# Kernel optimization log

Measured on AMD Instinct MI355X. Metric: run time of the kernel, lower is better.

## Reference

```python
import jax, jax.numpy as jnp
import numpy as np

N = 32768          # tokens per modal
TOKEN_DIM = 1024
HID_DIM = 1024
SENSE_DIM = 256
K = 512            # centroids (shared size across modals)


def setup_inputs() -> dict:
    key = jax.random.key(0)
    ks = jax.random.split(key, 10)
    s = 0.02
    return {
        "text_emb": jax.random.normal(ks[0], (N, TOKEN_DIM), jnp.float32),
        "image_emb": jax.random.normal(ks[1], (N, TOKEN_DIM), jnp.float32),
        "text_W1": jax.random.normal(ks[2], (TOKEN_DIM, HID_DIM), jnp.float32) * s,
        "text_W2": jax.random.normal(ks[3], (HID_DIM, HID_DIM), jnp.float32) * s,
        "text_W3": jax.random.normal(ks[4], (HID_DIM, SENSE_DIM), jnp.float32) * s,
        "image_W1": jax.random.normal(ks[5], (TOKEN_DIM, HID_DIM), jnp.float32) * s,
        "image_W2": jax.random.normal(ks[6], (HID_DIM, HID_DIM), jnp.float32) * s,
        "image_W3": jax.random.normal(ks[7], (HID_DIM, SENSE_DIM), jnp.float32) * s,
        "centroids_raw": jax.random.uniform(ks[8], (K, SENSE_DIM), jnp.float32),
    }


def _sense_map(x, W1, W2, W3):
    # Linear(bias=False)+Tanh x3
    h = jnp.tanh(x @ W1)
    h = jnp.tanh(h @ W2)
    return jnp.tanh(h @ W3)  # [N, sense_dim]


def _assign(se, centroids):
    # squared distance [K, N] via expansion (same math as broadcast-subtract)
    c2 = jnp.sum(centroids * centroids, axis=1)[:, None]      # [K,1]
    e2 = jnp.sum(se * se, axis=1)[None, :]                     # [1,N]
    sqdist = c2 + e2 - 2.0 * (centroids @ se.T)                # [K,N]
    # torch argmax over (sqdist.T == min) picks first min -> argmin first occurrence
    return jnp.argmin(sqdist, axis=0)                          # [N] int


def reference(text_emb, image_emb, text_W1, text_W2, text_W3,
              image_W1, image_W2, image_W3, centroids_raw):
    centroids = jnp.tanh(centroids_raw)
    se_t = _sense_map(text_emb, text_W1, text_W2, text_W3)
    se_i = _sense_map(image_emb, image_W1, image_W2, image_W3)
    sc_t = _assign(se_t, centroids)
    sc_i = _assign(se_i, centroids)

    sense_embeddings = jnp.concatenate([se_t, se_i], axis=0)   # [2N, sense_dim]
    sense_class = jnp.concatenate([sc_t, sc_i], axis=0)        # [2N]
    word_class = jnp.concatenate([jnp.zeros((N,), jnp.int32),
                                  jnp.ones((N,), jnp.int32)])

    # ragged per-sense grouping represented jit-compatibly as a stable sort
    # permutation + per-sense counts (per modal)
    order_t = jnp.argsort(sc_t, stable=True)
    order_i = jnp.argsort(sc_i, stable=True)
    counts_t = jnp.zeros((K,), jnp.int32).at[sc_t].add(1)
    counts_i = jnp.zeros((K,), jnp.int32).at[sc_i].add(1)

    return (centroids, sense_embeddings, word_class, sense_class,
            order_t, counts_t, order_i, counts_i)
```

## Files before the change

kernel.cpp:

```cpp
#include <hip/hip_runtime.h>
#include <math.h>

#define NTOK 32768
typedef unsigned short ushort_t;

#define OFF_CENT 0
#define OFF_SE   131072
#define OFF_WC   16908288
#define OFF_SC   16973824
#define OFF_OT   17039360
#define OFF_CT   17072128
#define OFF_OI   17072640
#define OFF_CI   17105408

typedef __attribute__((ext_vector_type(8))) short short8v;
typedef __attribute__((ext_vector_type(4))) float f32x4;

__device__ __forceinline__ float dot4(float4 a, float4 b){
    return a.x*b.x + a.y*b.y + a.z*b.z + a.w*b.w;
}

__device__ __forceinline__ ushort_t f2bf(float x){
    unsigned int u = __float_as_uint(x);
    unsigned int r = (u + 0x7fffu + ((u >> 16) & 1u)) >> 16;
    return (ushort_t)r;
}
__device__ __forceinline__ float bf2f(ushort_t h){
    return __uint_as_float(((unsigned int)h) << 16);
}

__device__ __forceinline__ void gload16(const void* g, void* l){
    __builtin_amdgcn_global_load_lds(
        (const __attribute__((address_space(1))) void*)g,
        (__attribute__((address_space(3))) void*)l,
        16, 0, 0);
}

__device__ __forceinline__ void cvt8(float4 a, float4 b, short8v& h, short8v& l){
    float x[8] = {a.x, a.y, a.z, a.w, b.x, b.y, b.z, b.w};
    #pragma unroll
    for (int i = 0; i < 8; ++i) {
        ushort_t hh = f2bf(x[i]);
        h[i] = (short)hh;
        l[i] = (short)f2bf(x[i] - bf2f(hh));
    }
}

__global__ __launch_bounds__(64) void k_cent(const float* __restrict__ raw,
                                             float* __restrict__ out,
                                             float* __restrict__ c2,
                                             ushort_t* __restrict__ ch,
                                             ushort_t* __restrict__ cl)
{
    int c = blockIdx.x, l = threadIdx.x;
    float4 v = *(const float4*)(raw + (size_t)c*256 + l*4);
    float4 t;
    t.x = tanhf(v.x); t.y = tanhf(v.y); t.z = tanhf(v.z); t.w = tanhf(v.w);
    *(float4*)(out + OFF_CENT + (size_t)c*256 + l*4) = t;
    ushort4 h = make_ushort4(f2bf(t.x), f2bf(t.y), f2bf(t.z), f2bf(t.w));
    ushort4 lo = make_ushort4(f2bf(t.x - bf2f(h.x)), f2bf(t.y - bf2f(h.y)),
                              f2bf(t.z - bf2f(h.z)), f2bf(t.w - bf2f(h.w)));
    *(ushort4*)(ch + (size_t)c*256 + l*4) = h;
    *(ushort4*)(cl + (size_t)c*256 + l*4) = lo;
    float s = dot4(t, t);
    #pragma unroll
    for (int off = 32; off > 0; off >>= 1) s += __shfl_down(s, off);
    if (l == 0) c2[c] = s;
}

__global__ __launch_bounds__(256) void k_esplit(const float* __restrict__ x,
                                                ushort_t* __restrict__ hi,
                                                ushort_t* __restrict__ lo,
                                                long n4)
{
    long g = (long)blockIdx.x*256 + threadIdx.x;
    if (g >= n4) return;
    float4 v = ((const float4*)x)[g];
    ushort_t h0 = f2bf(v.x), h1 = f2bf(v.y), h2 = f2bf(v.z), h3 = f2bf(v.w);
    ushort4 h = make_ushort4(h0, h1, h2, h3);
    ushort4 l = make_ushort4(f2bf(v.x - bf2f(h0)), f2bf(v.y - bf2f(h1)),
                             f2bf(v.z - bf2f(h2)), f2bf(v.w - bf2f(h3)));
    ((ushort4*)hi)[g] = h;
    ((ushort4*)lo)[g] = l;
}

__device__ __forceinline__ void wsplit_tile(const float* __restrict__ W,
                                            ushort_t* __restrict__ Wt_hi,
                                            ushort_t* __restrict__ Wt_lo,
                                            int K, int N, int bx, int by)
{
    __shared__ float t[32][33];
    int k0 = by*32, n0 = bx*32;
    int tx = threadIdx.x & 31, ty = threadIdx.x >> 5;
    #pragma unroll
    for (int r = 0; r < 4; ++r)
        t[ty + r*8][tx] = W[(size_t)(k0 + ty + r*8)*N + n0 + tx];
    __syncthreads();
    #pragma unroll
    for (int r = 0; r < 4; ++r) {
        int n = ty + r*8;
        float x = t[tx][n];
        ushort_t h = f2bf(x);
        Wt_hi[(size_t)(n0+n)*K + k0 + tx] = h;
        Wt_lo[(size_t)(n0+n)*K + k0 + tx] = f2bf(x - bf2f(h));
    }
}

__global__ __launch_bounds__(256) void k_prep(
    const float* __restrict__ W1t, const float* __restrict__ W2t, const float* __restrict__ W3t,
    const float* __restrict__ W1i, const float* __restrict__ W2i, const float* __restrict__ W3i,
    ushort_t* __restrict__ wreg, float* __restrict__ out)
{
    const size_t WM = 4*1048576 + 2*262144;
    int b = blockIdx.x;
    if (b >= 4608) {
        int g = (b - 4608)*256 + threadIdx.x;
        float v = (g*4 < NTOK) ? 0.f : 1.f;
        ((float4*)(out + OFF_WC))[g] = make_float4(v, v, v, v);
        return;
    }
    int m = b / 2304;
    int r = b % 2304;
    ushort_t* base = wreg + (size_t)m*WM;
    const float* Ws[3][2] = {{W1t, W1i}, {W2t, W2i}, {W3t, W3i}};
    if (r < 1024) {
        wsplit_tile(Ws[0][m], base, base + 1048576, 1024, 1024, r % 32, r / 32);
    } else if (r < 2048) {
        int r2 = r - 1024;
        wsplit_tile(Ws[1][m], base + 2*1048576, base + 3*1048576, 1024, 1024, r2 % 32, r2 / 32);
    } else {
        int r3 = r - 2048;
        wsplit_tile(Ws[2][m], base + 4*1048576, base + 4*1048576 + 262144, 1024, 256, r3 % 8, r3 / 8);
    }
}

__global__ __launch_bounds__(512, 2) void k_gemm_l1(
    const float* __restrict__ Af, const ushort_t* __restrict__ Bt_hi,
    ushort_t* __restrict__ C_hi, ushort_t* __restrict__ C_lo,
    unsigned bDelta, int N)
{
    __shared__ ushort_t lds[65536];

    const int tid  = threadIdx.x;
    const int wave = tid >> 6, lane = tid & 63;
    const int wr = wave >> 2, wc = wave & 3;
    const int fr = lane & 15, fq = lane >> 4;

    int nwg = gridDim.x;
    int id = blockIdx.x;
    if (!(nwg & 7)) { int cpx = nwg >> 3; id = (id & 7)*cpx + (id >> 3); }
    const int nx = N >> 8;
    const int n0 = (id % nx) * 256;
    const int m0 = (id / nx) * 256;

    const int srow0 = tid >> 2;
    const int qx = (tid & 3) ^ ((srow0 >> 1) & 3);

    const float* fA0 = Af + (size_t)(m0 + srow0) * 1024 + qx*8;
    const float* fA1 = fA0 + 131072;
    const unsigned offB0 = (unsigned)(n0 + srow0) * 1024u + (unsigned)qx * 8u;
    const ushort_t* pB0  = Bt_hi + offB0;
    const ushort_t* pB1  = pB0 + 131072u;
    const ushort_t* pB0l = pB0 + bDelta;
    const ushort_t* pB1l = pB1 + bDelta;
    const unsigned ldsS0 = (unsigned)wave * 512u;
    const unsigned ldsS1 = ldsS0 + 4096u;
    const unsigned wOff  = ldsS0 + (unsigned)lane * 8u;

    const unsigned fb = (unsigned)fr*32u + (unsigned)((fq ^ ((fr >> 1) & 3)) * 8);
    const ushort_t* p0 = lds + fb;
    const ushort_t* p1 = p0 + 32768u;

    f32x4 acc[8][4] = {};

#define STGB(KT, WB) { \
    unsigned wb_ = (unsigned)(WB) * 32768u; \
    gload16(pB0  + (KT), lds + wb_ + 16384u + ldsS0); \
    gload16(pB1  + (KT), lds + wb_ + 16384u + ldsS1); \
    gload16(pB0l + (KT), lds + wb_ + 24576u + ldsS0); \
    gload16(pB1l + (KT), lds + wb_ + 24576u + ldsS1); \
}
#define RA1(P, hl, i) (*(const short8v*)((P) + (hl)*8192u + (unsigned)wr*4096u + (unsigned)(i)*512u))
#define RB1(P, hl, j) (*(const short8v*)((P) + 16384u + (hl)*8192u + (unsigned)wc*2048u + (unsigned)(j)*512u))
#define MM16(A8, B8, C4) __builtin_amdgcn_mfma_f32_16x16x32_bf16(A8, B8, C4, 0, 0, 0)

    {
        float4 a00 = *(const float4*)(fA0);
        float4 a01 = *(const float4*)(fA0 + 4);
        float4 a10 = *(const float4*)(fA1);
        float4 a11 = *(const float4*)(fA1 + 4);
        STGB(0, 0);
        short8v h0, l0, h1, l1;
        cvt8(a00, a01, h0, l0);
        cvt8(a10, a11, h1, l1);
        *(short8v*)(lds + wOff)          = h0;
        *(short8v*)(lds + 4096u + wOff)  = h1;
        *(short8v*)(lds + 8192u + wOff)  = l0;
        *(short8v*)(lds + 12288u + wOff) = l1;
    }
    __syncthreads();

    #pragma unroll 1
    for (int kt = 0; kt < 1024; kt += 32) {
        const int par = (kt >> 5) & 1;
        const ushort_t* cp = par ? p1 : p0;
        const bool pf = (kt + 32) < 1024;

        float4 a00, a01, a10, a11;
        if (pf) {
            a00 = *(const float4*)(fA0 + kt + 32);
            a01 = *(const float4*)(fA0 + kt + 36);
            a10 = *(const float4*)(fA1 + kt + 32);
            a11 = *(const float4*)(fA1 + kt + 36);
            STGB(kt + 32, par ^ 1);
        }

        short8v bh0 = RB1(cp,0,0), bl0 = RB1(cp,1,0);
        short8v bh1 = RB1(cp,0,1), bl1 = RB1(cp,1,1);
        short8v bh2 = RB1(cp,0,2), bl2 = RB1(cp,1,2);
        short8v bh3 = RB1(cp,0,3), bl3 = RB1(cp,1,3);

        __builtin_amdgcn_s_setprio(1);
        #pragma unroll
        for (int i = 0; i < 8; ++i) {
            short8v ah = RA1(cp,0,i), al = RA1(cp,1,i);
            acc[i][0] = MM16(ah, bh0, acc[i][0]);
            acc[i][1] = MM16(ah, bh1, acc[i][1]);
            acc[i][2] = MM16(ah, bh2, acc[i][2]);
            acc[i][3] = MM16(ah, bh3, acc[i][3]);
            acc[i][0] = MM16(ah, bl0, acc[i][0]);
            acc[i][1] = MM16(ah, bl1, acc[i][1]);
            acc[i][2] = MM16(ah, bl2, acc[i][2]);
            acc[i][3] = MM16(ah, bl3, acc[i][3]);
            acc[i][0] = MM16(al, bh0, acc[i][0]);
            acc[i][1] = MM16(al, bh1, acc[i][1]);
            acc[i][2] = MM16(al, bh2, acc[i][2]);
            acc[i][3] = MM16(al, bh3, acc[i][3]);
        }
        __builtin_amdgcn_s_setprio(0);

        if (pf) {
            unsigned wb = (unsigned)(par ^ 1) * 32768u;
            short8v h0, l0, h1, l1;
            cvt8(a00, a01, h0, l0);
            cvt8(a10, a11, h1, l1);
            *(short8v*)(lds + wb + wOff)          = h0;
            *(short8v*)(lds + wb + 4096u + wOff)  = h1;
            *(short8v*)(lds + wb + 8192u + wOff)  = l0;
            *(short8v*)(lds + wb + 12288u + wOff) = l1;
        }
        __syncthreads();
    }

    #pragma unroll
    for (int i = 0; i < 8; ++i)
        #pragma unroll
        for (int j = 0; j < 4; ++j)
            #pragma unroll
            for (int r = 0; r < 4; ++r) {
                int row = m0 + wr*128 + i*16 + fq*4 + r;
                int col = n0 + wc*64 + j*16 + fr;
                float t = tanhf(acc[i][j][r]);
                size_t idx = (size_t)row*N + col;
                ushort_t h = f2bf(t);
                C_hi[idx] = h;
                C_lo[idx] = f2bf(t - bf2f(h));
            }
#undef STGB
#undef RA1
#undef RB1
#undef MM16
}

__global__ __launch_bounds__(512, 2) void k_gemm_mfma256(
    const ushort_t* __restrict__ A_hi, const ushort_t* __restrict__ Bt_hi,
    ushort_t* __restrict__ C_hi, ushort_t* __restrict__ C_lo,
    unsigned aDelta, unsigned bDelta, int N)
{
    __shared__ ushort_t lds[65536];

    const int tid  = threadIdx.x;
    const int wave = tid >> 6, lane = tid & 63;
    const int wr = wave >> 2, wc = wave & 3;
    const int fr = lane & 15, fq = lane >> 4;

    int nwg = gridDim.x;
    int id = blockIdx.x;
    if (!(nwg & 7)) { int cpx = nwg >> 3; id = (id & 7)*cpx + (id >> 3); }
    const int nx = N >> 8;
    const int n0 = (id % nx) * 256;
    const int m0 = (id / nx) * 256;

    const int srow0 = tid >> 2;
    const int qx = (tid & 3) ^ ((srow0 >> 1) & 3);

    const unsigned offA0 = (unsigned)(m0 + srow0) * 1024u + (unsigned)qx * 8u;
    const unsigned offB0 = (unsigned)(n0 + srow0) * 1024u + (unsigned)qx * 8u;
    const ushort_t* pA0  = A_hi + offA0;
    const ushort_t* pA1  = pA0 + 131072u;
    const ushort_t* pA0l = pA0 + aDelta;
    const ushort_t* pA1l = pA1 + aDelta;
    const ushort_t* pB0  = Bt_hi + offB0;
    const ushort_t* pB1  = pB0 + 131072u;
    const ushort_t* pB0l = pB0 + bDelta;
    const ushort_t* pB1l = pB1 + bDelta;
    const unsigned ldsS0 = (unsigned)wave * 512u;
    const unsigned ldsS1 = ldsS0 + 4096u;

    const unsigned fb = (unsigned)fr*32u + (unsigned)((fq ^ ((fr >> 1) & 3)) * 8);
    const ushort_t* p0 = lds + fb;
    const ushort_t* p1 = p0 + 32768u;

    f32x4 acc[8][4] = {};

#define STG(KT, WB) { \
    unsigned wb_ = (unsigned)(WB) * 32768u; \
    gload16(pA0  + (KT), lds + wb_ +           ldsS0); \
    gload16(pA1  + (KT), lds + wb_ +           ldsS1); \
    gload16(pA0l + (KT), lds + wb_ +  8192u +  ldsS0); \
    gload16(pA1l + (KT), lds + wb_ +  8192u +  ldsS1); \
    gload16(pB0  + (KT), lds + wb_ + 16384u +  ldsS0); \
    gload16(pB1  + (KT), lds + wb_ + 16384u +  ldsS1); \
    gload16(pB0l + (KT), lds + wb_ + 24576u +  ldsS0); \
    gload16(pB1l + (KT), lds + wb_ + 24576u +  ldsS1); \
}
#define RA(P, hl, i) (*(const short8v*)((P) + (hl)*8192u + (unsigned)wr*4096u + (unsigned)(i)*512u))
#define RB(P, hl, j) (*(const short8v*)((P) + 16384u + (hl)*8192u + (unsigned)wc*2048u + (unsigned)(j)*512u))
#define MM16(A8, B8, C4) __builtin_amdgcn_mfma_f32_16x16x32_bf16(A8, B8, C4, 0, 0, 0)

    STG(0, 0);
    __syncthreads();

    #pragma unroll 1
    for (int kt = 0; kt < 1024; kt += 32) {
        const int par = (kt >> 5) & 1;
        const ushort_t* cp = par ? p1 : p0;

        short8v bh0 = RB(cp,0,0), bl0 = RB(cp,1,0);
        short8v bh1 = RB(cp,0,1), bl1 = RB(cp,1,1);
        short8v bh2 = RB(cp,0,2), bl2 = RB(cp,1,2);
        short8v bh3 = RB(cp,0,3), bl3 = RB(cp,1,3);

        if (kt + 32 < 1024) STG(kt + 32, par ^ 1);

        __builtin_amdgcn_s_setprio(1);
        #pragma unroll
        for (int i = 0; i < 8; ++i) {
            short8v ah = RA(cp,0,i), al = RA(cp,1,i);
            acc[i][0] = MM16(ah, bh0, acc[i][0]);
            acc[i][1] = MM16(ah, bh1, acc[i][1]);
            acc[i][2] = MM16(ah, bh2, acc[i][2]);
            acc[i][3] = MM16(ah, bh3, acc[i][3]);
            acc[i][0] = MM16(ah, bl0, acc[i][0]);
            acc[i][1] = MM16(ah, bl1, acc[i][1]);
            acc[i][2] = MM16(ah, bl2, acc[i][2]);
            acc[i][3] = MM16(ah, bl3, acc[i][3]);
            acc[i][0] = MM16(al, bh0, acc[i][0]);
            acc[i][1] = MM16(al, bh1, acc[i][1]);
            acc[i][2] = MM16(al, bh2, acc[i][2]);
            acc[i][3] = MM16(al, bh3, acc[i][3]);
        }
        __builtin_amdgcn_s_setprio(0);

        __syncthreads();
    }

    #pragma unroll
    for (int i = 0; i < 8; ++i)
        #pragma unroll
        for (int j = 0; j < 4; ++j)
            #pragma unroll
            for (int r = 0; r < 4; ++r) {
                int row = m0 + wr*128 + i*16 + fq*4 + r;
                int col = n0 + wc*64 + j*16 + fr;
                float t = tanhf(acc[i][j][r]);
                size_t idx = (size_t)row*N + col;
                ushort_t h = f2bf(t);
                C_hi[idx] = h;
                C_lo[idx] = f2bf(t - bf2f(h));
            }
#undef STG
#undef RA
#undef RB
#undef MM16
}

__global__ __launch_bounds__(256, 2) void k_gemm_mfma(
    const ushort_t* __restrict__ A_hi, const ushort_t* __restrict__ A_lo,
    const ushort_t* __restrict__ Bt_hi, const ushort_t* __restrict__ Bt_lo,
    ushort_t* __restrict__ C_hi, ushort_t* __restrict__ C_lo,
    float* __restrict__ Cf,
    int N)
{
    __shared__ ushort_t lds[32768];

    const int tid  = threadIdx.x;
    const int wave = tid >> 6, lane = tid & 63;
    const int wr = wave >> 1, wc = wave & 1;
    const int fr = lane & 15, fq = lane >> 4;

    int nwg = gridDim.x * gridDim.y;
    int id = blockIdx.y * gridDim.x + blockIdx.x;
    if (!(nwg & 7)) { int cpx = nwg >> 3; id = (id & 7)*cpx + (id >> 3); }
    const int m0 = (id / gridDim.x) * 128, n0 = (id % gridDim.x) * 128;

    const int sl = lane >> 2;
    const int sq = (lane & 3) ^ ((sl >> 1) & 3);
    const unsigned ga0 = (unsigned)(m0 + wave*32 + sl) * 1024u + (unsigned)sq * 8u;
    const unsigned gb0 = (unsigned)(n0 + wave*32 + sl) * 1024u + (unsigned)sq * 8u;
    const ushort_t* pa0 = A_hi  + ga0;       const ushort_t* pa1 = pa0 + 16384u;
    const ushort_t* pal0 = A_lo + ga0;       const ushort_t* pal1 = pal0 + 16384u;
    const ushort_t* pb0 = Bt_hi + gb0;       const ushort_t* pb1 = pb0 + 16384u;
    const ushort_t* pbl0 = Bt_lo + gb0;      const ushort_t* pbl1 = pbl0 + 16384u;
    const unsigned sl0 = (unsigned)wave * 1024u;
    const unsigned sl1 = sl0 + 512u;

    const unsigned fb = (unsigned)fr*32u + (unsigned)((fq ^ ((fr >> 1) & 3)) * 8);
    const ushort_t* q0 = lds + fb;
    const ushort_t* q1 = q0 + 16384u;

    f32x4 acc[4][4] = {};

#define STG3(KT, WB) { \
    unsigned wb_ = (unsigned)(WB) * 16384u; \
    gload16(pa0  + (KT), lds + wb_ +           sl0); \
    gload16(pa1  + (KT), lds + wb_ +           sl1); \
    gload16(pal0 + (KT), lds + wb_ +  4096u +  sl0); \
    gload16(pal1 + (KT), lds + wb_ +  4096u +  sl1); \
    gload16(pb0  + (KT), lds + wb_ +  8192u +  sl0); \
    gload16(pb1  + (KT), lds + wb_ +  8192u +  sl1); \
    gload16(pbl0 + (KT), lds + wb_ + 12288u +  sl0); \
    gload16(pbl1 + (KT), lds + wb_ + 12288u +  sl1); \
}
#define RA3(P, hl, i) (*(const short8v*)((P) + (hl)*4096u + (unsigned)wr*2048u + (unsigned)(i)*512u))
#define RB3(P, hl, j) (*(const short8v*)((P) + 8192u + (hl)*4096u + (unsigned)wc*2048u + (unsigned)(j)*512u))
#define MM16(A8, B8, C4) __builtin_amdgcn_mfma_f32_16x16x32_bf16(A8, B8, C4, 0, 0, 0)

    STG3(0, 0);
    __syncthreads();

    #pragma unroll 1
    for (int kt = 0; kt < 1024; kt += 32) {
        const int par = (kt >> 5) & 1;
        const ushort_t* cp = par ? q1 : q0;

        short8v bh0 = RB3(cp,0,0), bl0 = RB3(cp,1,0);
        short8v bh1 = RB3(cp,0,1), bl1 = RB3(cp,1,1);
        short8v bh2 = RB3(cp,0,2), bl2 = RB3(cp,1,2);
        short8v bh3 = RB3(cp,0,3), bl3 = RB3(cp,1,3);

        if (kt + 32 < 1024) STG3(kt + 32, par ^ 1);

        __builtin_amdgcn_s_setprio(1);
        #pragma unroll
        for (int i = 0; i < 4; ++i) {
            short8v ah = RA3(cp,0,i), al = RA3(cp,1,i);
            acc[i][0] = MM16(ah, bh0, acc[i][0]);
            acc[i][1] = MM16(ah, bh1, acc[i][1]);
            acc[i][2] = MM16(ah, bh2, acc[i][2]);
            acc[i][3] = MM16(ah, bh3, acc[i][3]);
            acc[i][0] = MM16(ah, bl0, acc[i][0]);
            acc[i][1] = MM16(ah, bl1, acc[i][1]);
            acc[i][2] = MM16(ah, bl2, acc[i][2]);
            acc[i][3] = MM16(ah, bl3, acc[i][3]);
            acc[i][0] = MM16(al, bh0, acc[i][0]);
            acc[i][1] = MM16(al, bh1, acc[i][1]);
            acc[i][2] = MM16(al, bh2, acc[i][2]);
            acc[i][3] = MM16(al, bh3, acc[i][3]);
        }
        __builtin_amdgcn_s_setprio(0);

        __syncthreads();
    }

    #pragma unroll
    for (int i = 0; i < 4; ++i)
        #pragma unroll
        for (int j = 0; j < 4; ++j)
            #pragma unroll
            for (int r = 0; r < 4; ++r) {
                int row = m0 + wr*64 + i*16 + fq*4 + r;
                int col = n0 + wc*64 + j*16 + fr;
                float t = tanhf(acc[i][j][r]);
                size_t idx = (size_t)row*N + col;
                if (Cf) Cf[idx] = t;
                if (C_hi) {
                    ushort_t h = f2bf(t);
                    C_hi[idx] = h;
                    C_lo[idx] = f2bf(t - bf2f(h));
                }
            }
#undef STG3
#undef RA3
#undef RB3
#undef MM16
}

__global__ __launch_bounds__(256) void k_assign_mfma(
    const ushort_t* __restrict__ SEh, const ushort_t* __restrict__ SEl,
    const ushort_t* __restrict__ ch, const ushort_t* __restrict__ cl,
    const float* __restrict__ c2,
    int* __restrict__ sc, float* __restrict__ out_w,
    int* __restrict__ blockHist)
{
    __shared__ ushort_t lds[16384];
    __shared__ float c2s[512];
    __shared__ float redD[128][2];
    __shared__ int   redI[128][2];

    const int modal = blockIdx.y;
    const int t0 = blockIdx.x * 128;
    const int tid  = threadIdx.x;
    const int wave = tid >> 6, lane = tid & 63;
    const int wr = wave >> 1, wc = wave & 1;
    const int fr = lane & 15, fq = lane >> 4;

    const ushort_t* seh = SEh + (size_t)modal * NTOK * 256;
    const ushort_t* sel = SEl + (size_t)modal * NTOK * 256;

    c2s[tid] = c2[tid];
    c2s[tid + 256] = c2[tid + 256];

    int srow[2], sq[2], slbase[2];
    #pragma unroll
    for (int r = 0; r < 2; ++r) {
        int row = wave*32 + r*16 + (lane >> 2);
        srow[r]   = row;
        sq[r]     = (lane & 3) ^ ((row >> 1) & 3);
        slbase[r] = wave*1024 + r*512;
    }

    float bd[16]; int bi[16];
    #pragma unroll
    for (int s = 0; s < 16; ++s) { bd[s] = 3.4e38f; bi[s] = 0; }

    for (int j = 0; j < 4; ++j) {
        f32x4 acc[4][4] = {};
        for (int kt = 0; kt < 256; kt += 32) {
            __syncthreads();
            #pragma unroll
            for (int r = 0; r < 2; ++r) {
                size_t ga = (size_t)(t0 + srow[r]) * 256 + kt + sq[r]*8;
                size_t gc = (size_t)(j*128 + srow[r]) * 256 + kt + sq[r]*8;
                gload16(seh + ga, lds          + slbase[r]);
                gload16(sel + ga, lds + 4096   + slbase[r]);
                gload16(ch  + gc, lds + 8192   + slbase[r]);
                gload16(cl  + gc, lds + 12288  + slbase[r]);
            }
            __syncthreads();

            short8v ah[4], al[4], bh[4], bl[4];
            #pragma unroll
            for (int i = 0; i < 4; ++i) {
                int rowa = wr*64 + i*16 + fr;
                int offa = rowa*32 + ((fq ^ ((rowa >> 1) & 3)) * 8);
                ah[i] = *(const short8v*)(lds + offa);
                al[i] = *(const short8v*)(lds + 4096 + offa);
                int rowb = wc*64 + i*16 + fr;
                int offb = rowb*32 + ((fq ^ ((rowb >> 1) & 3)) * 8);
                bh[i] = *(const short8v*)(lds + 8192 + offb);
                bl[i] = *(const short8v*)(lds + 12288 + offb);
            }
            #pragma unroll
            for (int i = 0; i < 4; ++i)
                #pragma unroll
                for (int jj = 0; jj < 4; ++jj) {
                    acc[i][jj] = __builtin_amdgcn_mfma_f32_16x16x32_bf16(ah[i], bh[jj], acc[i][jj], 0, 0, 0);
                    acc[i][jj] = __builtin_amdgcn_mfma_f32_16x16x32_bf16(ah[i], bl[jj], acc[i][jj], 0, 0, 0);
                    acc[i][jj] = __builtin_amdgcn_mfma_f32_16x16x32_bf16(al[i], bh[jj], acc[i][jj], 0, 0, 0);
                }
        }
        #pragma unroll
        for (int i = 0; i < 4; ++i)
            #pragma unroll
            for (int jj = 0; jj < 4; ++jj) {
                int col = j*128 + wc*64 + jj*16 + fr;
                float cc = c2s[col];
                #pragma unroll
                for (int r = 0; r < 4; ++r) {
                    float d = cc - 2.f * acc[i][jj][r];
                    int s = i*4 + r;
                    if (d < bd[s]) { bd[s] = d; bi[s] = col; }
                }
            }
    }

    #pragma unroll
    for (int s = 0; s < 16; ++s) {
        #pragma unroll
        for (int off = 1; off < 16; off <<= 1) {
            float od = __shfl_xor(bd[s], off);
            int   oi = __shfl_xor(bi[s], off);
            if (od < bd[s] || (od == bd[s] && oi < bi[s])) { bd[s] = od; bi[s] = oi; }
        }
    }
    if (fr == 0) {
        #pragma unroll
        for (int i = 0; i < 4; ++i)
            #pragma unroll
            for (int r = 0; r < 4; ++r) {
                int tl = wr*64 + i*16 + fq*4 + r;
                redD[tl][wc] = bd[i*4 + r];
                redI[tl][wc] = bi[i*4 + r];
            }
    }
    __syncthreads();
    if (tid < 128) {
        float d0 = redD[tid][0], d1 = redD[tid][1];
        int   i0 = redI[tid][0], i1 = redI[tid][1];
        if (d1 < d0 || (d1 == d0 && i1 < i0)) { d0 = d1; i0 = i1; }
        int g = t0 + tid;
        sc[modal*NTOK + g] = i0;
        out_w[OFF_SC + (size_t)modal*NTOK + g] = (float)i0;
        atomicAdd(&blockHist[(modal*128 + (g >> 8))*512 + i0], 1);
    }
}

__global__ __launch_bounds__(256) void k_assign(
    const float* __restrict__ out_ro,
    const float* __restrict__ c2,
    int* __restrict__ sc,
    float* __restrict__ out_w,
    int* __restrict__ blockHist)
{
    const int modal = blockIdx.y;
    const int tok0 = blockIdx.x * 64;
    const float* se   = out_ro + OFF_SE + (size_t)modal * NTOK * 256;
    const float* cent = out_ro + OFF_CENT;

    __shared__ float4 se4[64][64];
    __shared__ float4 ct4[64][64];

    const int tid = threadIdx.x;
    const int tt = tid & 15, cc = tid >> 4;

    {
        int rbase = tid >> 6;
        int d4 = tid & 63;
        #pragma unroll
        for (int i = 0; i < 16; ++i) {
            int t = i*4 + rbase;
            float4 v = *(const float4*)(se + (size_t)(tok0 + t)*256 + d4*4);
            se4[t][d4 ^ (t >> 2)] = v;
        }
    }
    __syncthreads();

    float e2r[4];
    #pragma unroll
    for (int k2 = 0; k2 < 4; ++k2) {
        float s = 0.f;
        for (int d4 = 0; d4 < 64; ++d4) {
            float4 v = se4[4*tt + k2][d4 ^ tt];
            s += dot4(v, v);
        }
        e2r[k2] = s;
    }

    float bd[4]; int bi[4];
    #pragma unroll
    for (int k2 = 0; k2 < 4; ++k2) { bd[k2] = 3.4e38f; bi[k2] = 0; }

    for (int ctile = 0; ctile < 8; ++ctile) {
        int c0 = ctile * 64;
        {
            int rbase = tid >> 6;
            int d4 = tid & 63;
            #pragma unroll
            for (int i = 0; i < 16; ++i) {
                int r = i*4 + rbase;
                float4 v = *(const float4*)(cent + (size_t)(c0 + r)*256 + d4*4);
                ct4[r][d4 ^ (r >> 2)] = v;
            }
        }
        __syncthreads();

        float accd[4][4];
        #pragma unroll
        for (int a = 0; a < 4; ++a)
            #pragma unroll
            for (int b = 0; b < 4; ++b) accd[a][b] = 0.f;

        for (int d4 = 0; d4 < 64; ++d4) {
            float4 sv[4], cv[4];
            #pragma unroll
            for (int k2 = 0; k2 < 4; ++k2) sv[k2] = se4[4*tt + k2][d4 ^ tt];
            #pragma unroll
            for (int jx = 0; jx < 4; ++jx) cv[jx] = ct4[4*cc + jx][d4 ^ cc];
            #pragma unroll
            for (int k2 = 0; k2 < 4; ++k2)
                #pragma unroll
                for (int jx = 0; jx < 4; ++jx)
                    accd[k2][jx] += dot4(sv[k2], cv[jx]);
        }

        #pragma unroll
        for (int jx = 0; jx < 4; ++jx) {
            int cidx = c0 + 4*cc + jx;
            float cj = c2[cidx];
            #pragma unroll
            for (int k2 = 0; k2 < 4; ++k2) {
                float d = cj + e2r[k2] - 2.f * accd[k2][jx];
                if (d < bd[k2]) { bd[k2] = d; bi[k2] = cidx; }
            }
        }
        __syncthreads();
    }

    float* red_d = (float*)ct4;
    int*   red_i = (int*)ct4 + 64*17;
    #pragma unroll
    for (int k2 = 0; k2 < 4; ++k2) {
        red_d[(4*tt + k2)*17 + cc] = bd[k2];
        red_i[(4*tt + k2)*17 + cc] = bi[k2];
    }
    __syncthreads();
    if (tid < 64) {
        float b = red_d[tid*17]; int ix = red_i[tid*17];
        #pragma unroll
        for (int q = 1; q < 16; ++q) {
            float d = red_d[tid*17 + q]; int i2 = red_i[tid*17 + q];
            if (d < b || (d == b && i2 < ix)) { b = d; ix = i2; }
        }
        int g = tok0 + tid;
        sc[modal*NTOK + g] = ix;
        out_w[OFF_SC + (size_t)modal*NTOK + g] = (float)ix;
        atomicAdd(&blockHist[(modal*128 + (g >> 8))*512 + ix], 1);
    }
}

__global__ __launch_bounds__(512) void k_scan(const int* __restrict__ blockHist,
                                              int* __restrict__ blockBase,
                                              int* __restrict__ classBase,
                                              float* __restrict__ out)
{
    int modal = blockIdx.x;
    int c = threadIdx.x;
    int run = 0;
    for (int b = 0; b < 128; ++b) {
        int idx = (modal*128 + b)*512 + c;
        blockBase[idx] = run;
        run += blockHist[idx];
    }
    float* cnt = out + (modal ? OFF_CI : OFF_CT);
    cnt[c] = (float)run;

    __shared__ int s[512];
    s[c] = run;
    __syncthreads();
    int total = run;
    for (int off = 1; off < 512; off <<= 1) {
        int v = 0;
        if (c >= off) v = s[c - off];
        __syncthreads();
        s[c] += v;
        __syncthreads();
    }
    classBase[modal*512 + c] = s[c] - total;
}

__global__ __launch_bounds__(256) void k_scatter(const int* __restrict__ sc,
                                                 const int* __restrict__ blockBase,
                                                 const int* __restrict__ classBase,
                                                 float* __restrict__ out)
{
    int modal = blockIdx.y, blk = blockIdx.x, tid = threadIdx.x;
    __shared__ int cls[256];
    int t = blk*256 + tid;
    int c = sc[modal*NTOK + t];
    cls[tid] = c;
    __syncthreads();
    int rank = 0;
    for (int j = 0; j < tid; ++j) rank += (cls[j] == c) ? 1 : 0;
    int pos = classBase[modal*512 + c] + blockBase[(modal*128 + blk)*512 + c] + rank;
    float* oo = out + (modal ? OFF_OI : OFF_OT);
    oo[pos] = (float)t;
}

extern "C" void kernel_launch(void* const* d_in, const int* in_sizes, int n_in,
                              void* d_out, int out_size, void* d_ws, size_t ws_size,
                              hipStream_t stream)
{
    const float* text_emb  = (const float*)d_in[0];
    const float* image_emb = (const float*)d_in[1];
    const float* W[2][3] = {
        {(const float*)d_in[2], (const float*)d_in[3], (const float*)d_in[4]},
        {(const float*)d_in[5], (const float*)d_in[6], (const float*)d_in[7]}
    };
    const float* cent_raw = (const float*)d_in[8];
    float* out = (float*)d_out;
    char* w = (char*)d_ws;

    int*   sc        = (int*)w;
    int*   blockHist = (int*)(w + 0x40000);
    int*   blockBase = (int*)(w + 0xC0000);
    int*   classBase = (int*)(w + 0x140000);
    float* c2        = (float*)(w + 0x141000);
    ushort_t* cent_h = (ushort_t*)(w + 0x142000);
    ushort_t* cent_l = (ushort_t*)(w + 0x182000);

    ushort_t* wreg = (ushort_t*)(w + 0x200000);
    const size_t WM = 4*1048576 + 2*262144;

    ushort_t* SEh = (ushort_t*)(w + 0x1400000);
    ushort_t* SEl = (ushort_t*)(w + 0x3400000);

    bool mfmaAssign = true;
    size_t actoff = 0x5400000;
    int Mc = 0;
    for (int c = NTOK; c >= 256; c >>= 1)
        if (actoff + (size_t)c*8192 <= ws_size) { Mc = c; break; }
    if (Mc == 0) {
        mfmaAssign = false;
        actoff = 0x1400000;
        for (int c = NTOK; c >= 256; c >>= 1)
            if (actoff + (size_t)c*8192 <= ws_size) { Mc = c; break; }
        if (Mc == 0) Mc = 256;
    }
    ushort_t* act = (ushort_t*)(w + actoff);

    hipMemsetAsync(blockHist, 0, 2*128*512*sizeof(int), stream);

    k_cent<<<dim3(512), dim3(64), 0, stream>>>(cent_raw, out, c2, cent_h, cent_l);
    k_prep<<<dim3(4672), dim3(256), 0, stream>>>(
        W[0][0], W[0][1], W[0][2], W[1][0], W[1][1], W[1][2], wreg, out);

    for (int m = 0; m < 2; ++m) {
        const float* emb = m ? image_emb : text_emb;
        ushort_t* w1h = wreg + (size_t)m*WM;
        ushort_t* w2h = w1h + 2*1048576;
        ushort_t* w3h = w1h + 4*1048576;
        ushort_t* w3l = w3h + 262144;

        ushort_t* Ah = act;
        ushort_t* Al = Ah + (size_t)Mc*1024;
        ushort_t* Hh = Al + (size_t)Mc*1024;
        ushort_t* Hl = Hh + (size_t)Mc*1024;

        for (int s0 = 0; s0 < NTOK; s0 += Mc) {
            k_gemm_l1<<<dim3((Mc/256)*4), dim3(512), 0, stream>>>(
                emb + (size_t)s0*1024, w1h, Hh, Hl, 1048576u, 1024);
            k_gemm_mfma256<<<dim3((Mc/256)*4), dim3(512), 0, stream>>>(
                Hh, w2h, Ah, Al, (unsigned)Mc*1024u, 1048576u, 1024);
            ushort_t* seh_ptr = mfmaAssign ? SEh + ((size_t)m*NTOK + s0)*256 : nullptr;
            ushort_t* sel_ptr = mfmaAssign ? SEl + ((size_t)m*NTOK + s0)*256 : nullptr;
            k_gemm_mfma<<<dim3(2, Mc/128), dim3(256), 0, stream>>>(
                Ah, Al, w3h, w3l, seh_ptr, sel_ptr,
                out + OFF_SE + ((size_t)m*NTOK + s0)*256, 256);
        }
    }

    if (mfmaAssign) {
        k_assign_mfma<<<dim3(256, 2), dim3(256), 0, stream>>>(
            SEh, SEl, cent_h, cent_l, c2, sc, out, blockHist);
    } else {
        k_assign<<<dim3(512, 2), dim3(256), 0, stream>>>(out, c2, sc, out, blockHist);
    }
    k_scan   <<<dim3(2),      dim3(512), 0, stream>>>(blockHist, blockBase, classBase, out);
    k_scatter<<<dim3(128, 2), dim3(256), 0, stream>>>(sc, blockBase, classBase, out);
}
```

Measured before the change: 1.030 ms.

## Double-buffer assign MFMA loads, fuse centroid prep, parallelize histogram scan

The assign kernel now runs one flattened 32-step loop with double-buffered LDS, so global-to-LDS loads for the next tile overlap the MFMA work on the current one and one barrier per step is removed. Centroid tanh and split is folded into k_prep as extra blocks, removing a separate launch. The serial 128-step per-class scan is split into a parallel wave-shuffle scan across blocks followed by a small class-prefix kernel. LDS use in the assign kernel doubles, which may lower occupancy.

```diff
diff --git a/kernel.cpp b/kernel.cpp
--- a/kernel.cpp
+++ b/kernel.cpp
@@ -44,28 +44,6 @@
         h[i] = (short)hh;
         l[i] = (short)f2bf(x[i] - bf2f(hh));
     }
-}
-
-__global__ __launch_bounds__(64) void k_cent(const float* __restrict__ raw,
-                                             float* __restrict__ out,
-                                             float* __restrict__ c2,
-                                             ushort_t* __restrict__ ch,
-                                             ushort_t* __restrict__ cl)
-{
-    int c = blockIdx.x, l = threadIdx.x;
-    float4 v = *(const float4*)(raw + (size_t)c*256 + l*4);
-    float4 t;
-    t.x = tanhf(v.x); t.y = tanhf(v.y); t.z = tanhf(v.z); t.w = tanhf(v.w);
-    *(float4*)(out + OFF_CENT + (size_t)c*256 + l*4) = t;
-    ushort4 h = make_ushort4(f2bf(t.x), f2bf(t.y), f2bf(t.z), f2bf(t.w));
-    ushort4 lo = make_ushort4(f2bf(t.x - bf2f(h.x)), f2bf(t.y - bf2f(h.y)),
-                              f2bf(t.z - bf2f(h.z)), f2bf(t.w - bf2f(h.w)));
-    *(ushort4*)(ch + (size_t)c*256 + l*4) = h;
-    *(ushort4*)(cl + (size_t)c*256 + l*4) = lo;
-    float s = dot4(t, t);
-    #pragma unroll
-    for (int off = 32; off > 0; off >>= 1) s += __shfl_down(s, off);
-    if (l == 0) c2[c] = s;
 }
 
 __global__ __launch_bounds__(256) void k_esplit(const float* __restrict__ x,
@@ -109,10 +87,30 @@
 __global__ __launch_bounds__(256) void k_prep(
     const float* __restrict__ W1t, const float* __restrict__ W2t, const float* __restrict__ W3t,
     const float* __restrict__ W1i, const float* __restrict__ W2i, const float* __restrict__ W3i,
-    ushort_t* __restrict__ wreg, float* __restrict__ out)
+    ushort_t* __restrict__ wreg, float* __restrict__ out,
+    const float* __restrict__ cent_raw, float* __restrict__ c2,
+    ushort_t* __restrict__ ch, ushort_t* __restrict__ cl)
 {
     const size_t WM = 4*1048576 + 2*262144;
     int b = blockIdx.x;
+    if (b >= 4672) {
+        int c = (b - 4672)*4 + (threadIdx.x >> 6);
+        int l = threadIdx.x & 63;
+        float4 v = *(const float4*)(cent_raw + (size_t)c*256 + l*4);
+        float4 t;
+        t.x = tanhf(v.x); t.y = tanhf(v.y); t.z = tanhf(v.z); t.w = tanhf(v.w);
+        *(float4*)(out + OFF_CENT + (size_t)c*256 + l*4) = t;
+        ushort4 h = make_ushort4(f2bf(t.x), f2bf(t.y), f2bf(t.z), f2bf(t.w));
+        ushort4 lo = make_ushort4(f2bf(t.x - bf2f(h.x)), f2bf(t.y - bf2f(h.y)),
+                                  f2bf(t.z - bf2f(h.z)), f2bf(t.w - bf2f(h.w)));
+        *(ushort4*)(ch + (size_t)c*256 + l*4) = h;
+        *(ushort4*)(cl + (size_t)c*256 + l*4) = lo;
+        float s = dot4(t, t);
+        #pragma unroll
+        for (int off = 32; off > 0; off >>= 1) s += __shfl_down(s, off);
+        if (l == 0) c2[c] = s;
+        return;
+    }
     if (b >= 4608) {
         int g = (b - 4608)*256 + threadIdx.x;
         float v = (g*4 < NTOK) ? 0.f : 1.f;
@@ -503,7 +501,7 @@
     int* __restrict__ sc, float* __restrict__ out_w,
     int* __restrict__ blockHist)
 {
-    __shared__ ushort_t lds[16384];
+    __shared__ ushort_t lds[32768];
     __shared__ float c2s[512];
     __shared__ float redD[128][2];
     __shared__ int   redI[128][2];
@@ -521,69 +519,92 @@
     c2s[tid] = c2[tid];
     c2s[tid + 256] = c2[tid + 256];
 
-    int srow[2], sq[2], slbase[2];
-    #pragma unroll
-    for (int r = 0; r < 2; ++r) {
-        int row = wave*32 + r*16 + (lane >> 2);
-        srow[r]   = row;
-        sq[r]     = (lane & 3) ^ ((row >> 1) & 3);
-        slbase[r] = wave*1024 + r*512;
-    }
+    const int sl = lane >> 2;
+    const int sq = (lane & 3) ^ ((sl >> 1) & 3);
+    const unsigned sA = (unsigned)(t0 + wave*32 + sl) * 256u + (unsigned)sq * 8u;
+    const unsigned sC = (unsigned)(wave*32 + sl) * 256u + (unsigned)sq * 8u;
+    const ushort_t* pse0 = seh + sA;   const ushort_t* pse1 = pse0 + 4096u;
+    const ushort_t* psl0 = sel + sA;   const ushort_t* psl1 = psl0 + 4096u;
+    const ushort_t* pch0 = ch + sC;    const ushort_t* pch1 = pch0 + 4096u;
+    const ushort_t* pcl0 = cl + sC;    const ushort_t* pcl1 = pcl0 + 4096u;
+    const unsigned d0 = (unsigned)wave * 1024u;
+    const unsigned d1 = d0 + 512u;
+
+#define STA(S, BUF) { \
+    int j_ = (S) >> 3; unsigned kt_ = (unsigned)((S) & 7) * 32u; \
+    unsigned bb = (unsigned)(BUF) * 16384u; \
+    unsigned co = (unsigned)j_*32768u + kt_; \
+    gload16(pse0 + kt_, lds + bb +           d0); \
+    gload16(pse1 + kt_, lds + bb +           d1); \
+    gload16(psl0 + kt_, lds + bb +  4096u +  d0); \
+    gload16(psl1 + kt_, lds + bb +  4096u +  d1); \
+    gload16(pch0 + co,  lds + bb +  8192u +  d0); \
+    gload16(pch1 + co,  lds + bb +  8192u +  d1); \
+    gload16(pcl0 + co,  lds + bb + 12288u +  d0); \
+    gload16(pcl1 + co,  lds + bb + 12288u +  d1); \
+}
 
     float bd[16]; int bi[16];
     #pragma unroll
     for (int s = 0; s < 16; ++s) { bd[s] = 3.4e38f; bi[s] = 0; }
 
-    for (int j = 0; j < 4; ++j) {
-        f32x4 acc[4][4] = {};
-        for (int kt = 0; kt < 256; kt += 32) {
-            __syncthreads();
-            #pragma unroll
-            for (int r = 0; r < 2; ++r) {
-                size_t ga = (size_t)(t0 + srow[r]) * 256 + kt + sq[r]*8;
-                size_t gc = (size_t)(j*128 + srow[r]) * 256 + kt + sq[r]*8;
-                gload16(seh + ga, lds          + slbase[r]);
-                gload16(sel + ga, lds + 4096   + slbase[r]);
-                gload16(ch  + gc, lds + 8192   + slbase[r]);
-                gload16(cl  + gc, lds + 12288  + slbase[r]);
+    STA(0, 0);
+    __syncthreads();
+
+    f32x4 acc[4][4];
+    #pragma unroll 1
+    for (int s = 0; s < 32; ++s) {
+        const int j = s >> 3;
+        const ushort_t* cp = lds + (unsigned)(s & 1) * 16384u;
+
+        if ((s & 7) == 0) {
+            #pragma unroll
+            for (int i = 0; i < 4; ++i)
+                #pragma unroll
+                for (int jj = 0; jj < 4; ++jj) acc[i][jj] = (f32x4){0.f,0.f,0.f,0.f};
+        }
+
+        if (s + 1 < 32) STA(s + 1, (s & 1) ^ 1);
+
+        short8v ah[4], al[4], bh[4], bl[4];
+        #pragma unroll
+        for (int i = 0; i < 4; ++i) {
+            int rowa = wr*64 + i*16 + fr;
+            int offa = rowa*32 + ((fq ^ ((rowa >> 1) & 3)) * 8);
+            ah[i] = *(const short8v*)(cp + offa);
+            al[i] = *(const short8v*)(cp + 4096 + offa);
+            int rowb = wc*64 + i*16 + fr;
+            int offb = rowb*32 + ((fq ^ ((rowb >> 1) & 3)) * 8);
+            bh[i] = *(const short8v*)(cp + 8192 + offb);
+            bl[i] = *(const short8v*)(cp + 12288 + offb);
+        }
+        #pragma unroll
+        for (int i = 0; i < 4; ++i)
+            #pragma unroll
+            for (int jj = 0; jj < 4; ++jj) {
+                acc[i][jj] = __builtin_amdgcn_mfma_f32_16x16x32_bf16(ah[i], bh[jj], acc[i][jj], 0, 0, 0);
+                acc[i][jj] = __builtin_amdgcn_mfma_f32_16x16x32_bf16(ah[i], bl[jj], acc[i][jj], 0, 0, 0);
+                acc[i][jj] = __builtin_amdgcn_mfma_f32_16x16x32_bf16(al[i], bh[jj], acc[i][jj], 0, 0, 0);
             }
-            __syncthreads();
-
-            short8v ah[4], al[4], bh[4], bl[4];
-            #pragma unroll
-            for (int i = 0; i < 4; ++i) {
-                int rowa = wr*64 + i*16 + fr;
-                int offa = rowa*32 + ((fq ^ ((rowa >> 1) & 3)) * 8);
-                ah[i] = *(const short8v*)(lds + offa);
-                al[i] = *(const short8v*)(lds + 4096 + offa);
-                int rowb = wc*64 + i*16 + fr;
-                int offb = rowb*32 + ((fq ^ ((rowb >> 1) & 3)) * 8);
-                bh[i] = *(const short8v*)(lds + 8192 + offb);
-                bl[i] = *(const short8v*)(lds + 12288 + offb);
-            }
+
+        if ((s & 7) == 7) {
             #pragma unroll
             for (int i = 0; i < 4; ++i)
                 #pragma unroll
                 for (int jj = 0; jj < 4; ++jj) {
-                    acc[i][jj] = __builtin_amdgcn_mfma_f32_16x16x32_bf16(ah[i], bh[jj], acc[i][jj], 0, 0, 0);
-                    acc[i][jj] = __builtin_amdgcn_mfma_f32_16x16x32_bf16(ah[i], bl[jj], acc[i][jj], 0, 0, 0);
-                    acc[i][jj] = __builtin_amdgcn_mfma_f32_16x16x32_bf16(al[i], bh[jj], acc[i][jj], 0, 0, 0);
+                    int col = j*128 + wc*64 + jj*16 + fr;
+                    float cc = c2s[col];
+                    #pragma unroll
+                    for (int r = 0; r < 4; ++r) {
+                        float d = cc - 2.f * acc[i][jj][r];
+                        int si = i*4 + r;
+                        if (d < bd[si]) { bd[si] = d; bi[si] = col; }
+                    }
                 }
         }
-        #pragma unroll
-        for (int i = 0; i < 4; ++i)
-            #pragma unroll
-            for (int jj = 0; jj < 4; ++jj) {
-                int col = j*128 + wc*64 + jj*16 + fr;
-                float cc = c2s[col];
-                #pragma unroll
-                for (int r = 0; r < 4; ++r) {
-                    float d = cc - 2.f * acc[i][jj][r];
-                    int s = i*4 + r;
-                    if (d < bd[s]) { bd[s] = d; bi[s] = col; }
-                }
-            }
-    }
+        __syncthreads();
+    }
+#undef STA
 
     #pragma unroll
     for (int s = 0; s < 16; ++s) {
@@ -606,9 +627,9 @@
     }
     __syncthreads();
     if (tid < 128) {
-        float d0 = redD[tid][0], d1 = redD[tid][1];
+        float dd0 = redD[tid][0], dd1 = redD[tid][1];
         int   i0 = redI[tid][0], i1 = redI[tid][1];
-        if (d1 < d0 || (d1 == d0 && i1 < i0)) { d0 = d1; i0 = i1; }
+        if (dd1 < dd0 || (dd1 == dd0 && i1 < i0)) { dd0 = dd1; i0 = i1; }
         int g = t0 + tid;
         sc[modal*NTOK + g] = i0;
         out_w[OFF_SC + (size_t)modal*NTOK + g] = (float)i0;
@@ -729,26 +750,38 @@
     }
 }
 
-__global__ __launch_bounds__(512) void k_scan(const int* __restrict__ blockHist,
-                                              int* __restrict__ blockBase,
-                                              int* __restrict__ classBase,
-                                              float* __restrict__ out)
+__global__ __launch_bounds__(128) void k_scan1(const int* __restrict__ blockHist,
+                                               int* __restrict__ blockBase,
+                                               int* __restrict__ classTot)
+{
+    int c = blockIdx.x, modal = blockIdx.y, t = threadIdx.x;
+    __shared__ int wsum;
+    int v = blockHist[(modal*128 + t)*512 + c];
+    int incl = v;
+    #pragma unroll
+    for (int off = 1; off < 64; off <<= 1) {
+        int u = __shfl_up(incl, off);
+        if ((t & 63) >= off) incl += u;
+    }
+    if (t == 63) wsum = incl;
+    __syncthreads();
+    if (t >= 64) incl += wsum;
+    blockBase[(modal*128 + t)*512 + c] = incl - v;
+    if (t == 127) classTot[modal*512 + c] = incl;
+}
+
+__global__ __launch_bounds__(512) void k_scan2(int* __restrict__ classBase,
+                                               float* __restrict__ out)
 {
     int modal = blockIdx.x;
     int c = threadIdx.x;
-    int run = 0;
-    for (int b = 0; b < 128; ++b) {
-        int idx = (modal*128 + b)*512 + c;
-        blockBase[idx] = run;
-        run += blockHist[idx];
-    }
+    int total = classBase[modal*512 + c];
     float* cnt = out + (modal ? OFF_CI : OFF_CT);
-    cnt[c] = (float)run;
+    cnt[c] = (float)total;
 
     __shared__ int s[512];
-    s[c] = run;
-    __syncthreads();
-    int total = run;
+    s[c] = total;
+    __syncthreads();
     for (int off = 1; off < 512; off <<= 1) {
         int v = 0;
         if (c >= off) v = s[c - off];
@@ -821,9 +854,9 @@
 
     hipMemsetAsync(blockHist, 0, 2*128*512*sizeof(int), stream);
 
-    k_cent<<<dim3(512), dim3(64), 0, stream>>>(cent_raw, out, c2, cent_h, cent_l);
-    k_prep<<<dim3(4672), dim3(256), 0, stream>>>(
-        W[0][0], W[0][1], W[0][2], W[1][0], W[1][1], W[1][2], wreg, out);
+    k_prep<<<dim3(4800), dim3(256), 0, stream>>>(
+        W[0][0], W[0][1], W[0][2], W[1][0], W[1][1], W[1][2], wreg, out,
+        cent_raw, c2, cent_h, cent_l);
 
     for (int m = 0; m < 2; ++m) {
         const float* emb = m ? image_emb : text_emb;
@@ -856,6 +889,7 @@
     } else {
         k_assign<<<dim3(512, 2), dim3(256), 0, stream>>>(out, c2, sc, out, blockHist);
     }
-    k_scan   <<<dim3(2),      dim3(512), 0, stream>>>(blockHist, blockBase, classBase, out);
+    k_scan1  <<<dim3(512, 2), dim3(128), 0, stream>>>(blockHist, blockBase, classBase);
+    k_scan2  <<<dim3(2),      dim3(512), 0, stream>>>(classBase, out);
     k_scatter<<<dim3(128, 2), dim3(256), 0, stream>>>(sc, blockBase, classBase, out);
 }
```

New measurement: 1.034 ms, median of 3. About the same (+0.3%).
